# Performance work log

Hardware: AMD Instinct MI355X
Metric: run time of the kernel (lower is better)

The kernel has to match this reference:

```python
import jax, jax.numpy as jnp
import numpy as np

DIM_SED = 256
DIM_DOA = 256
DIM_ATTN = 256
NUM_HEADS = 8
HEAD_DIM = DIM_ATTN // NUM_HEADS
SCALE = HEAD_DIM ** -0.5
B, N_SED, N_DOA = 2, 2048, 2048


def setup_inputs() -> dict:
    key = jax.random.key(0)
    ks = jax.random.split(key, 8)
    s = lambda fan_in: 1.0 / np.sqrt(fan_in)
    return {
        "x_sed": jax.random.normal(ks[0], (B, N_SED, DIM_SED), jnp.float32),
        "x_doa": jax.random.normal(ks[1], (B, N_DOA, DIM_DOA), jnp.float32),
        # nn.Linear stores weight as [out, in]; we keep [in, out] for x @ W
        "W_sed_in": jax.random.uniform(ks[2], (DIM_SED, 2 * DIM_ATTN), jnp.float32, -s(DIM_SED), s(DIM_SED)),
        "W_doa_in": jax.random.uniform(ks[3], (DIM_DOA, 2 * DIM_ATTN), jnp.float32, -s(DIM_DOA), s(DIM_DOA)),
        "W_sed_out": jax.random.uniform(ks[4], (DIM_ATTN, DIM_SED), jnp.float32, -s(DIM_ATTN), s(DIM_ATTN)),
        "b_sed_out": jax.random.uniform(ks[5], (DIM_SED,), jnp.float32, -s(DIM_ATTN), s(DIM_ATTN)),
        "W_doa_out": jax.random.uniform(ks[6], (DIM_ATTN, DIM_DOA), jnp.float32, -s(DIM_ATTN), s(DIM_ATTN)),
        "b_doa_out": jax.random.uniform(ks[7], (DIM_DOA,), jnp.float32, -s(DIM_ATTN), s(DIM_ATTN)),
    }


def _split_heads(rv, B, N):
    # rv: [B, N, 2*DIM_ATTN] -> r, v each [B, H, N, hd]
    rv = rv.reshape(B, N, 2, NUM_HEADS, HEAD_DIM).transpose(2, 0, 3, 1, 4)
    return rv[0], rv[1]


def reference(x_sed, x_doa, W_sed_in, W_doa_in, W_sed_out, b_sed_out, W_doa_out, b_doa_out):
    B_, Ns, _ = x_sed.shape
    _, Nd, _ = x_doa.shape
    r_sed, v_sed = _split_heads(x_sed @ W_sed_in, B_, Ns)  # [B,H,Ns,hd]
    r_doa, v_doa = _split_heads(x_doa @ W_doa_in, B_, Nd)  # [B,H,Nd,hd]

    # Shared score matrix, softmaxed in both directions (dropout = identity, eval mode)
    attn = jnp.einsum('bhsd,bhtd->bhst', r_sed, r_doa) * SCALE  # [B,H,Ns,Nd]
    attn_sed2doa = jax.nn.softmax(attn, axis=-1)               # row-wise
    attn_doa2sed = jax.nn.softmax(attn, axis=-2)               # col-wise (softmax of attn^T over last dim)

    x_sed_fused = jnp.einsum('bhst,bhtd->bhsd', attn_sed2doa, v_doa)
    x_sed_fused = x_sed_fused.transpose(0, 2, 1, 3).reshape(B_, Ns, DIM_ATTN)
    x_sed_fused = x_sed_fused @ W_sed_out + b_sed_out

    x_doa_fused = jnp.einsum('bhst,bhsd->bhtd', attn_doa2sed, v_sed)
    x_doa_fused = x_doa_fused.transpose(0, 2, 1, 3).reshape(B_, Nd, DIM_ATTN)
    x_doa_fused = x_doa_fused @ W_doa_out + b_doa_out
    return (x_sed_fused, x_doa_fused)
```

## Files before the change

### kernel.cpp

```cpp
#include <hip/hip_runtime.h>
#include <hip/hip_bf16.h>

typedef short short8 __attribute__((ext_vector_type(8)));
typedef float f32x4 __attribute__((ext_vector_type(4)));
typedef float f32x16 __attribute__((ext_vector_type(16)));
typedef unsigned int uint4v __attribute__((ext_vector_type(4)));
typedef unsigned short ushort_t;

__device__ inline ushort_t f2bf(float f) {
    union { float f; unsigned u; } x; x.f = f;
    unsigned r = x.u + 0x7fffu + ((x.u >> 16) & 1u);
    return (ushort_t)(r >> 16);
}
__device__ inline ushort_t f2bf_u(float x) {
    union { __hip_bfloat16 h; ushort_t u; } cv;
    cv.h = __float2bfloat16(x);
    return cv.u;
}
__device__ inline float bf2f(ushort_t u) {
    union { unsigned u; float f; } cv; cv.u = ((unsigned)u) << 16; return cv.f;
}

#define GLD_LDS16(src, dst)                                                  \
    __builtin_amdgcn_global_load_lds(                                        \
        (const __attribute__((address_space(1))) void*)(src),                \
        (__attribute__((address_space(3))) void*)(dst), 16, 0, 0)

#define RSQ 0.5050100f

__global__ __launch_bounds__(256) void prep_w_kernel(const float* __restrict__ w0,
                                                     const float* __restrict__ w1,
                                                     const float* __restrict__ w2,
                                                     const float* __restrict__ w3,
                                                     ushort_t* __restrict__ t0,
                                                     ushort_t* __restrict__ t1,
                                                     ushort_t* __restrict__ t2,
                                                     ushort_t* __restrict__ t3) {
    __shared__ float tile[64][65];
    int z = blockIdx.y;
    const float* W; ushort_t* T; int J;
    if (z == 0)      { W = w0; T = t0; J = 512; }
    else if (z == 1) { W = w1; T = t1; J = 512; }
    else if (z == 2) { W = w2; T = t2; J = 256; }
    else             { W = w3; T = t3; J = 256; }
    int ntj = J >> 6;
    int nt = ntj * 4;
    int tix = blockIdx.x;
    if (tix >= nt) return;
    int tj = tix % ntj, tk = tix / ntj;
    int j0 = tj * 64, k0 = tk * 64;
    int tid = threadIdx.x;

    int jj = (tid & 15) * 4, kk0 = tid >> 4;
    #pragma unroll
    for (int kk = kk0; kk < 64; kk += 16) {
        float4 v = *reinterpret_cast<const float4*>(&W[(size_t)(k0 + kk) * J + j0 + jj]);
        tile[kk][jj] = v.x; tile[kk][jj + 1] = v.y;
        tile[kk][jj + 2] = v.z; tile[kk][jj + 3] = v.w;
    }
    __syncthreads();
    int kk4 = (tid & 15) * 4, jj0 = tid >> 4;
    #pragma unroll
    for (int j2 = jj0; j2 < 64; j2 += 16) {
        ushort4 o;
        o.x = f2bf(tile[kk4][j2]);     o.y = f2bf(tile[kk4 + 1][j2]);
        o.z = f2bf(tile[kk4 + 2][j2]); o.w = f2bf(tile[kk4 + 3][j2]);
        *reinterpret_cast<ushort4*>(&T[(size_t)(j0 + j2) * 256 + k0 + kk4]) = o;
    }
}

__global__ __launch_bounds__(256) void gemm_in_kernel(
    const float* __restrict__ A0, const float* __restrict__ A1,
    const ushort_t* __restrict__ B0, const ushort_t* __restrict__ B1,
    ushort_t* __restrict__ R0, ushort_t* __restrict__ R1,
    ushort_t* __restrict__ V0, ushort_t* __restrict__ V1) {
    const float* A = blockIdx.z ? A1 : A0;
    const ushort_t* Bt = blockIdx.z ? B1 : B0;
    ushort_t* R = blockIdx.z ? R1 : R0;
    ushort_t* Vt = blockIdx.z ? V1 : V0;
    constexpr int K = 256;
    const int w = threadIdx.x >> 6, lane = threadIdx.x & 63;
    const int l16 = lane & 15, g = lane >> 4;
    const int m0 = blockIdx.x * 64 + w * 16;
    const int cb = blockIdx.y * 128;

    f32x4 acc[8] = {};
    const float* Ap = A + (size_t)(m0 + l16) * K + 8 * g;
    const ushort_t* Bp = Bt + (size_t)(cb + l16) * K + 8 * g;

    #pragma unroll
    for (int ks = 0; ks < K; ks += 32) {
        float4 af0 = *reinterpret_cast<const float4*>(Ap + ks);
        float4 af1 = *reinterpret_cast<const float4*>(Ap + ks + 4);
        short8 a;
        a[0] = (short)f2bf_u(af0.x); a[1] = (short)f2bf_u(af0.y);
        a[2] = (short)f2bf_u(af0.z); a[3] = (short)f2bf_u(af0.w);
        a[4] = (short)f2bf_u(af1.x); a[5] = (short)f2bf_u(af1.y);
        a[6] = (short)f2bf_u(af1.z); a[7] = (short)f2bf_u(af1.w);
        #pragma unroll
        for (int c = 0; c < 8; ++c) {
            short8 b = *reinterpret_cast<const short8*>(Bp + (size_t)c * 16 * K + ks);
            acc[c] = __builtin_amdgcn_mfma_f32_16x16x32_bf16(a, b, acc[c], 0, 0, 0);
        }
    }

    if (blockIdx.y < 2) {
        #pragma unroll
        for (int c = 0; c < 8; ++c) {
            int col = cb + c * 16 + l16;
            int h = col >> 5, d = col & 31;
            #pragma unroll
            for (int r = 0; r < 4; ++r) {
                int row = m0 + 4 * g + r;
                int bb = row >> 11, n = row & 2047;
                size_t base = (size_t)(bb * 8 + h) * 65536;
                int unit = ((n >> 5) * 4 + (d >> 4) * 2 + ((d >> 3) & 1)) * 32 + (n & 31);
                R[base + (size_t)unit * 8 + (d & 7)] = f2bf_u(acc[c][r] * RSQ);
            }
        }
    } else {
        #pragma unroll
        for (int c = 0; c < 8; ++c) {
            int colp = cb - 256 + c * 16 + l16;
            int h = colp >> 5, d = colp & 31;
            int row = m0 + 4 * g;
            int bb = row >> 11, n = row & 2047;
            size_t base = (size_t)(bb * 8 + h) * 65536;
            int nl = n & 31;
            int vh = nl >> 4, r4 = nl & 15;
            int hi2 = (r4 >> 2) & 1;
            int e0 = (r4 & 3) + 4 * (r4 >> 3);
            int unit = ((n >> 5) * 4 + vh * 2 + hi2) * 32 + d;
            ushort4 s;
            s.x = f2bf_u(acc[c][0]); s.y = f2bf_u(acc[c][1]);
            s.z = f2bf_u(acc[c][2]); s.w = f2bf_u(acc[c][3]);
            *reinterpret_cast<ushort4*>(Vt + base + (size_t)unit * 8 + e0) = s;
        }
    }
}

__global__ __launch_bounds__(512, 4) void attn_kernel(
    const ushort_t* __restrict__ rU_sed, const ushort_t* __restrict__ rU_doa,
    const ushort_t* __restrict__ vU_sed, const ushort_t* __restrict__ vU_doa,
    ushort_t* __restrict__ part,
    float* __restrict__ lpart) {
    __shared__ __align__(16) ushort_t smem[16384];

    const int bid = blockIdx.x;
    const int xcd = bid & 7, i = bid >> 3;
    const int stream = xcd * 4 + (i & 3);
    const int rest = i >> 2;
    const int qblk = rest & 7, kvh = rest >> 3;
    const int dir = stream >> 4, bh = stream & 15;

    const ushort_t* rQ = dir ? rU_doa : rU_sed;
    const ushort_t* rK = dir ? rU_sed : rU_doa;
    const ushort_t* vV = dir ? vU_sed : vU_doa;

    const int tid = threadIdx.x;
    const int w = tid >> 6, lane = tid & 63;
    const int l31 = lane & 31, hi = lane >> 5;
    const size_t sB = (size_t)bh * 65536;
    const int qbase = qblk * 256 + w * 32;

    const short8 qf0 = *reinterpret_cast<const short8*>(rQ + sB + (size_t)qbase * 32 + lane * 8);
    const short8 qf1 = *reinterpret_cast<const short8*>(rQ + sB + (size_t)qbase * 32 + 512 + lane * 8);

    const ushort_t* Kbase = rK + sB + (size_t)kvh * 32768;
    const ushort_t* Vbase = vV + sB + (size_t)kvh * 32768;
    const ushort_t* srcK = Kbase + tid * 8;
    const ushort_t* srcV = Vbase + tid * 8;
    const int dstK = w * 512;
    const int dstV = 4096 + w * 512;

    f32x16 acc = {};
    f32x4 lv = {};

    auto stage = [&](int t, int bufsel) {
        GLD_LDS16(srcK + (size_t)t * 4096, &smem[bufsel * 8192 + dstK]);
        GLD_LDS16(srcV + (size_t)t * 4096, &smem[bufsel * 8192 + dstV]);
    };

    int buf = 0;
    stage(0, 0);
    __syncthreads();

    for (int t = 0; t < 8; ++t) {
        if (t < 7) stage(t + 1, buf ^ 1);
        const ushort_t* KB = &smem[buf * 8192];
        const ushort_t* VB = &smem[buf * 8192 + 4096];
        #pragma unroll
        for (int s = 0; s < 4; ++s) {
            short8 kf0 = *reinterpret_cast<const short8*>(KB + s * 1024 + lane * 8);
            short8 kf1 = *reinterpret_cast<const short8*>(KB + s * 1024 + 512 + lane * 8);
            short8 vf0 = *reinterpret_cast<const short8*>(VB + s * 1024 + lane * 8);
            short8 vf1 = *reinterpret_cast<const short8*>(VB + s * 1024 + 512 + lane * 8);

            f32x16 z16 = {};
            f32x16 st = __builtin_amdgcn_mfma_f32_32x32x16_bf16(kf0, qf0, z16, 0, 0, 0);
            st = __builtin_amdgcn_mfma_f32_32x32x16_bf16(kf1, qf1, st, 0, 0, 0);

            float p[16];
            #pragma unroll
            for (int j = 0; j < 16; ++j) {
                p[j] = __builtin_amdgcn_exp2f(st[j]);
            }
            #pragma unroll
            for (int j = 0; j < 16; ++j) lv[j & 3] += p[j];

            unsigned pk[8];
            #pragma unroll
            for (int j = 0; j < 8; ++j) {
                asm("v_cvt_pk_bf16_f32 %0, %1, %2" : "=v"(pk[j]) : "v"(p[2 * j]), "v"(p[2 * j + 1]));
            }
            union { uint4v u; short8 s; } c1, c2;
            c1.u = uint4v{pk[0], pk[1], pk[2], pk[3]};
            c2.u = uint4v{pk[4], pk[5], pk[6], pk[7]};

            acc = __builtin_amdgcn_mfma_f32_32x32x16_bf16(vf0, c1.s, acc, 0, 0, 0);
            acc = __builtin_amdgcn_mfma_f32_32x32x16_bf16(vf1, c2.s, acc, 0, 0, 0);
        }
        __syncthreads();
        buf ^= 1;
    }

    float l = (lv[0] + lv[1]) + (lv[2] + lv[3]);
    l += __shfl_xor(l, 32);
    const int q = qbase + l31;
    const size_t prow = ((size_t)stream * 2 + kvh) * 2048 + q;
    if (lane < 32) lpart[prow] = l;
    ushort_t* pa = part + prow * 32;
    #pragma unroll
    for (int r = 0; r < 16; ++r) {
        int d = (r & 3) + 8 * (r >> 2) + 4 * hi;
        pa[d] = f2bf(acc[r]);
    }
}

__global__ __launch_bounds__(256) void gemm_out_kernel(
    const ushort_t* __restrict__ part, const float* __restrict__ lpart,
    const ushort_t* __restrict__ b0, const ushort_t* __restrict__ b1,
    float* __restrict__ c0, float* __restrict__ c1,
    const float* __restrict__ bias0, const float* __restrict__ bias1) {
    const int z = blockIdx.z;
    const ushort_t* Bt = z ? b1 : b0;
    float* C = z ? c1 : c0;
    const float* bias = z ? bias1 : bias0;
    constexpr int K = 256, N = 256;
    const int w = threadIdx.x >> 6, lane = threadIdx.x & 63;
    const int l16 = lane & 15, g = lane >> 4;
    const int m0 = blockIdx.x * 64 + w * 16;
    const int cb = blockIdx.y * 128;

    const int row = m0 + l16;
    const int bb = row >> 11, q = row & 2047;

    f32x4 acc[8] = {};
    const ushort_t* Bp = Bt + (size_t)(cb + l16) * K + 8 * g;
    #pragma unroll
    for (int it = 0; it < 8; ++it) {
        const int strm = z * 16 + bb * 8 + it;
        const size_t pr0 = ((size_t)strm * 2) * 2048 + q;
        float l0 = lpart[pr0], l1 = lpart[pr0 + 2048];
        float inv = 1.0f / (l0 + l1);
        const ushort_t* p0 = part + pr0 * 32 + 8 * g;
        const ushort_t* p1 = p0 + (size_t)2048 * 32;
        short8 pa = *reinterpret_cast<const short8*>(p0);
        short8 pb = *reinterpret_cast<const short8*>(p1);
        short8 a;
        #pragma unroll
        for (int e = 0; e < 8; ++e) {
            a[e] = (short)f2bf_u((bf2f((ushort_t)pa[e]) + bf2f((ushort_t)pb[e])) * inv);
        }
        #pragma unroll
        for (int c = 0; c < 8; ++c) {
            short8 b = *reinterpret_cast<const short8*>(Bp + (size_t)c * 16 * K + it * 32);
            acc[c] = __builtin_amdgcn_mfma_f32_16x16x32_bf16(a, b, acc[c], 0, 0, 0);
        }
    }
    #pragma unroll
    for (int c = 0; c < 8; ++c) {
        int col = cb + c * 16 + l16;
        #pragma unroll
        for (int r = 0; r < 4; ++r) {
            int orow = m0 + 4 * g + r;
            C[(size_t)orow * N + col] = acc[c][r] + bias[col];
        }
    }
}

extern "C" void kernel_launch(void* const* d_in, const int* in_sizes, int n_in,
                              void* d_out, int out_size, void* d_ws, size_t ws_size,
                              hipStream_t stream) {
    const float* x_sed     = (const float*)d_in[0];
    const float* x_doa     = (const float*)d_in[1];
    const float* W_sed_in  = (const float*)d_in[2];
    const float* W_doa_in  = (const float*)d_in[3];
    const float* W_sed_out = (const float*)d_in[4];
    const float* b_sed_out = (const float*)d_in[5];
    const float* W_doa_out = (const float*)d_in[6];
    const float* b_doa_out = (const float*)d_in[7];
    float* out = (float*)d_out;

    ushort_t* ws = (ushort_t*)d_ws;
    ushort_t* wt_si  = ws;
    ushort_t* wt_di  = wt_si  + 131072;
    ushort_t* wt_so  = wt_di  + 131072;
    ushort_t* wt_do  = wt_so  + 65536;
    ushort_t* rU_sed = wt_do  + 65536;
    ushort_t* rU_doa = rU_sed + 1048576;
    ushort_t* vU_sed = rU_doa + 1048576;
    ushort_t* vU_doa = vU_sed + 1048576;
    ushort_t* part   = vU_doa + 1048576;
    float*    lpart  = (float*)(part + 4194304);

    prep_w_kernel<<<dim3(32, 4), 256, 0, stream>>>(W_sed_in, W_doa_in, W_sed_out, W_doa_out,
                                                   wt_si, wt_di, wt_so, wt_do);
    gemm_in_kernel<<<dim3(64, 4, 2), 256, 0, stream>>>(x_sed, x_doa, wt_si, wt_di,
                                                       rU_sed, rU_doa, vU_sed, vU_doa);
    attn_kernel<<<dim3(512), 512, 0, stream>>>(rU_sed, rU_doa, vU_sed, vU_doa, part, lpart);
    gemm_out_kernel<<<dim3(64, 2, 2), 256, 0, stream>>>(part, lpart, wt_so, wt_do,
                                                        out, out + 1048576, b_sed_out, b_doa_out);
}
```

Measured before the change: 67.52 us.

## Double KV tile size and software-pipeline QK MFMA ahead of softmax-PV

Staged KV tiles double from 128 to 256 keys per step, so the loop runs 4 iterations with half as many barriers. Inside each tile, the QK^T MFMA for sub-block s is issued before the exp/convert/PV work of sub-block s-1, letting matrix ops overlap transcendental and convert work. Row sums now accumulate in a 16-wide vector, which avoids a serial add chain but costs more registers. LDS use doubles to 64 KB per block, which may reduce occupancy against the launch bound of 4 blocks.

```diff
diff --git a/kernel.cpp b/kernel.cpp
--- a/kernel.cpp
+++ b/kernel.cpp
@@ -144,7 +144,7 @@
     const ushort_t* __restrict__ vU_sed, const ushort_t* __restrict__ vU_doa,
     ushort_t* __restrict__ part,
     float* __restrict__ lpart) {
-    __shared__ __align__(16) ushort_t smem[16384];
+    __shared__ __align__(16) ushort_t smem[32768];
 
     const int bid = blockIdx.x;
     const int xcd = bid & 7, i = bid >> 3;
@@ -170,61 +170,70 @@
     const ushort_t* Vbase = vV + sB + (size_t)kvh * 32768;
     const ushort_t* srcK = Kbase + tid * 8;
     const ushort_t* srcV = Vbase + tid * 8;
-    const int dstK = w * 512;
-    const int dstV = 4096 + w * 512;
 
     f32x16 acc = {};
-    f32x4 lv = {};
+    f32x16 lvv = {};
 
     auto stage = [&](int t, int bufsel) {
-        GLD_LDS16(srcK + (size_t)t * 4096, &smem[bufsel * 8192 + dstK]);
-        GLD_LDS16(srcV + (size_t)t * 4096, &smem[bufsel * 8192 + dstV]);
+        const ushort_t* sk = srcK + (size_t)t * 8192;
+        const ushort_t* sv = srcV + (size_t)t * 8192;
+        ushort_t* dk = &smem[bufsel * 16384 + w * 512];
+        GLD_LDS16(sk,        dk);
+        GLD_LDS16(sk + 4096, dk + 4096);
+        GLD_LDS16(sv,        dk + 8192);
+        GLD_LDS16(sv + 4096, dk + 12288);
+    };
+
+    auto QK = [&](const ushort_t* KB, int s) -> f32x16 {
+        short8 kf0 = *reinterpret_cast<const short8*>(KB + s * 1024 + lane * 8);
+        short8 kf1 = *reinterpret_cast<const short8*>(KB + s * 1024 + 512 + lane * 8);
+        f32x16 z16 = {};
+        f32x16 st = __builtin_amdgcn_mfma_f32_32x32x16_bf16(kf0, qf0, z16, 0, 0, 0);
+        return __builtin_amdgcn_mfma_f32_32x32x16_bf16(kf1, qf1, st, 0, 0, 0);
+    };
+
+    auto FIN = [&](const ushort_t* VB, int s, f32x16 st) {
+        short8 vf0 = *reinterpret_cast<const short8*>(VB + s * 1024 + lane * 8);
+        short8 vf1 = *reinterpret_cast<const short8*>(VB + s * 1024 + 512 + lane * 8);
+        f32x16 pv;
+        #pragma unroll
+        for (int j = 0; j < 16; ++j) pv[j] = __builtin_amdgcn_exp2f(st[j]);
+        lvv += pv;
+        unsigned pk[8];
+        #pragma unroll
+        for (int j = 0; j < 8; ++j) {
+            asm("v_cvt_pk_bf16_f32 %0, %1, %2" : "=v"(pk[j]) : "v"(pv[2 * j]), "v"(pv[2 * j + 1]));
+        }
+        union { uint4v u; short8 s; } c1, c2;
+        c1.u = uint4v{pk[0], pk[1], pk[2], pk[3]};
+        c2.u = uint4v{pk[4], pk[5], pk[6], pk[7]};
+        acc = __builtin_amdgcn_mfma_f32_32x32x16_bf16(vf0, c1.s, acc, 0, 0, 0);
+        acc = __builtin_amdgcn_mfma_f32_32x32x16_bf16(vf1, c2.s, acc, 0, 0, 0);
     };
 
     int buf = 0;
     stage(0, 0);
     __syncthreads();
 
-    for (int t = 0; t < 8; ++t) {
-        if (t < 7) stage(t + 1, buf ^ 1);
-        const ushort_t* KB = &smem[buf * 8192];
-        const ushort_t* VB = &smem[buf * 8192 + 4096];
-        #pragma unroll
-        for (int s = 0; s < 4; ++s) {
-            short8 kf0 = *reinterpret_cast<const short8*>(KB + s * 1024 + lane * 8);
-            short8 kf1 = *reinterpret_cast<const short8*>(KB + s * 1024 + 512 + lane * 8);
-            short8 vf0 = *reinterpret_cast<const short8*>(VB + s * 1024 + lane * 8);
-            short8 vf1 = *reinterpret_cast<const short8*>(VB + s * 1024 + 512 + lane * 8);
-
-            f32x16 z16 = {};
-            f32x16 st = __builtin_amdgcn_mfma_f32_32x32x16_bf16(kf0, qf0, z16, 0, 0, 0);
-            st = __builtin_amdgcn_mfma_f32_32x32x16_bf16(kf1, qf1, st, 0, 0, 0);
-
-            float p[16];
-            #pragma unroll
-            for (int j = 0; j < 16; ++j) {
-                p[j] = __builtin_amdgcn_exp2f(st[j]);
-            }
-            #pragma unroll
-            for (int j = 0; j < 16; ++j) lv[j & 3] += p[j];
-
-            unsigned pk[8];
-            #pragma unroll
-            for (int j = 0; j < 8; ++j) {
-                asm("v_cvt_pk_bf16_f32 %0, %1, %2" : "=v"(pk[j]) : "v"(p[2 * j]), "v"(p[2 * j + 1]));
-            }
-            union { uint4v u; short8 s; } c1, c2;
-            c1.u = uint4v{pk[0], pk[1], pk[2], pk[3]};
-            c2.u = uint4v{pk[4], pk[5], pk[6], pk[7]};
-
-            acc = __builtin_amdgcn_mfma_f32_32x32x16_bf16(vf0, c1.s, acc, 0, 0, 0);
-            acc = __builtin_amdgcn_mfma_f32_32x32x16_bf16(vf1, c2.s, acc, 0, 0, 0);
-        }
+    for (int t = 0; t < 4; ++t) {
+        if (t < 3) stage(t + 1, buf ^ 1);
+        const ushort_t* KB = &smem[buf * 16384];
+        const ushort_t* VB = KB + 8192;
+        f32x16 st_p = QK(KB, 0);
+        #pragma unroll
+        for (int s = 1; s < 8; ++s) {
+            f32x16 st_n = QK(KB, s);
+            FIN(VB, s - 1, st_p);
+            st_p = st_n;
+        }
+        FIN(VB, 7, st_p);
         __syncthreads();
         buf ^= 1;
     }
 
-    float l = (lv[0] + lv[1]) + (lv[2] + lv[3]);
+    float l = 0.f;
+    #pragma unroll
+    for (int j = 0; j < 16; ++j) l += lvv[j];
     l += __shfl_xor(l, 32);
     const int q = qbase + l31;
     const size_t prow = ((size_t)stream * 2 + kvh) * 2048 + q;
```

After: 67.84 us. Within noise of the previous version (+0.5%).

## Split attention into 4 KV partitions with smaller 256-thread blocks

Applied to the files above, without the earlier changes.

The attention kernel changes from 512 blocks of 512 threads, each covering half the keys, to 2048 blocks of 256 threads, each covering a quarter of the keys over 128 queries. Staging issues four LDS loads per thread, and the exp and pack work is split into two halves to shorten register live ranges. The output GEMM now reduces four partial accumulators and four partial row sums. The aim is more parallelism and better latency hiding, at the cost of twice the partial-output traffic and a larger reduction in the output kernel.

```diff
diff --git a/kernel.cpp b/kernel.cpp
--- a/kernel.cpp
+++ b/kernel.cpp
@@ -139,7 +139,7 @@
     }
 }
 
-__global__ __launch_bounds__(512, 4) void attn_kernel(
+__global__ __launch_bounds__(256, 5) void attn_kernel(
     const ushort_t* __restrict__ rU_sed, const ushort_t* __restrict__ rU_doa,
     const ushort_t* __restrict__ vU_sed, const ushort_t* __restrict__ vU_doa,
     ushort_t* __restrict__ part,
@@ -150,7 +150,7 @@
     const int xcd = bid & 7, i = bid >> 3;
     const int stream = xcd * 4 + (i & 3);
     const int rest = i >> 2;
-    const int qblk = rest & 7, kvh = rest >> 3;
+    const int qblk = rest & 15, kvq = rest >> 4;
     const int dir = stream >> 4, bh = stream & 15;
 
     const ushort_t* rQ = dir ? rU_doa : rU_sed;
@@ -161,34 +161,37 @@
     const int w = tid >> 6, lane = tid & 63;
     const int l31 = lane & 31, hi = lane >> 5;
     const size_t sB = (size_t)bh * 65536;
-    const int qbase = qblk * 256 + w * 32;
+    const int qbase = qblk * 128 + w * 32;
 
     const short8 qf0 = *reinterpret_cast<const short8*>(rQ + sB + (size_t)qbase * 32 + lane * 8);
     const short8 qf1 = *reinterpret_cast<const short8*>(rQ + sB + (size_t)qbase * 32 + 512 + lane * 8);
 
-    const ushort_t* Kbase = rK + sB + (size_t)kvh * 32768;
-    const ushort_t* Vbase = vV + sB + (size_t)kvh * 32768;
+    const ushort_t* Kbase = rK + sB + (size_t)kvq * 16384;
+    const ushort_t* Vbase = vV + sB + (size_t)kvq * 16384;
     const ushort_t* srcK = Kbase + tid * 8;
     const ushort_t* srcV = Vbase + tid * 8;
-    const int dstK = w * 512;
-    const int dstV = 4096 + w * 512;
 
     f32x16 acc = {};
     f32x4 lv = {};
 
     auto stage = [&](int t, int bufsel) {
-        GLD_LDS16(srcK + (size_t)t * 4096, &smem[bufsel * 8192 + dstK]);
-        GLD_LDS16(srcV + (size_t)t * 4096, &smem[bufsel * 8192 + dstV]);
+        const ushort_t* sk = srcK + (size_t)t * 4096;
+        const ushort_t* sv = srcV + (size_t)t * 4096;
+        ushort_t* dk = &smem[bufsel * 8192 + w * 512];
+        GLD_LDS16(sk,        dk);
+        GLD_LDS16(sk + 2048, dk + 2048);
+        GLD_LDS16(sv,        dk + 4096);
+        GLD_LDS16(sv + 2048, dk + 6144);
     };
 
     int buf = 0;
     stage(0, 0);
     __syncthreads();
 
-    for (int t = 0; t < 8; ++t) {
-        if (t < 7) stage(t + 1, buf ^ 1);
+    for (int t = 0; t < 4; ++t) {
+        if (t < 3) stage(t + 1, buf ^ 1);
         const ushort_t* KB = &smem[buf * 8192];
-        const ushort_t* VB = &smem[buf * 8192 + 4096];
+        const ushort_t* VB = KB + 4096;
         #pragma unroll
         for (int s = 0; s < 4; ++s) {
             short8 kf0 = *reinterpret_cast<const short8*>(KB + s * 1024 + lane * 8);
@@ -200,25 +203,38 @@
             f32x16 st = __builtin_amdgcn_mfma_f32_32x32x16_bf16(kf0, qf0, z16, 0, 0, 0);
             st = __builtin_amdgcn_mfma_f32_32x32x16_bf16(kf1, qf1, st, 0, 0, 0);
 
-            float p[16];
-            #pragma unroll
-            for (int j = 0; j < 16; ++j) {
-                p[j] = __builtin_amdgcn_exp2f(st[j]);
+            short8 c1s, c2s;
+            {
+                float p[8]; unsigned pk[4];
+                #pragma unroll
+                for (int j = 0; j < 8; ++j) p[j] = __builtin_amdgcn_exp2f(st[j]);
+                #pragma unroll
+                for (int j = 0; j < 8; ++j) lv[j & 3] += p[j];
+                #pragma unroll
+                for (int j = 0; j < 4; ++j) {
+                    asm("v_cvt_pk_bf16_f32 %0, %1, %2" : "=v"(pk[j]) : "v"(p[2 * j]), "v"(p[2 * j + 1]));
+                }
+                union { uint4v u; short8 s; } cc;
+                cc.u = uint4v{pk[0], pk[1], pk[2], pk[3]};
+                c1s = cc.s;
             }
-            #pragma unroll
-            for (int j = 0; j < 16; ++j) lv[j & 3] += p[j];
-
-            unsigned pk[8];
-            #pragma unroll
-            for (int j = 0; j < 8; ++j) {
-                asm("v_cvt_pk_bf16_f32 %0, %1, %2" : "=v"(pk[j]) : "v"(p[2 * j]), "v"(p[2 * j + 1]));
+            {
+                float p[8]; unsigned pk[4];
+                #pragma unroll
+                for (int j = 0; j < 8; ++j) p[j] = __builtin_amdgcn_exp2f(st[8 + j]);
+                #pragma unroll
+                for (int j = 0; j < 8; ++j) lv[j & 3] += p[j];
+                #pragma unroll
+                for (int j = 0; j < 4; ++j) {
+                    asm("v_cvt_pk_bf16_f32 %0, %1, %2" : "=v"(pk[j]) : "v"(p[2 * j]), "v"(p[2 * j + 1]));
+                }
+                union { uint4v u; short8 s; } cc;
+                cc.u = uint4v{pk[0], pk[1], pk[2], pk[3]};
+                c2s = cc.s;
             }
-            union { uint4v u; short8 s; } c1, c2;
-            c1.u = uint4v{pk[0], pk[1], pk[2], pk[3]};
-            c2.u = uint4v{pk[4], pk[5], pk[6], pk[7]};
-
-            acc = __builtin_amdgcn_mfma_f32_32x32x16_bf16(vf0, c1.s, acc, 0, 0, 0);
-            acc = __builtin_amdgcn_mfma_f32_32x32x16_bf16(vf1, c2.s, acc, 0, 0, 0);
+
+            acc = __builtin_amdgcn_mfma_f32_32x32x16_bf16(vf0, c1s, acc, 0, 0, 0);
+            acc = __builtin_amdgcn_mfma_f32_32x32x16_bf16(vf1, c2s, acc, 0, 0, 0);
         }
         __syncthreads();
         buf ^= 1;
@@ -227,7 +243,7 @@
     float l = (lv[0] + lv[1]) + (lv[2] + lv[3]);
     l += __shfl_xor(l, 32);
     const int q = qbase + l31;
-    const size_t prow = ((size_t)stream * 2 + kvh) * 2048 + q;
+    const size_t prow = ((size_t)stream * 4 + kvq) * 2048 + q;
     if (lane < 32) lpart[prow] = l;
     ushort_t* pa = part + prow * 32;
     #pragma unroll
@@ -260,17 +276,20 @@
     #pragma unroll
     for (int it = 0; it < 8; ++it) {
         const int strm = z * 16 + bb * 8 + it;
-        const size_t pr0 = ((size_t)strm * 2) * 2048 + q;
-        float l0 = lpart[pr0], l1 = lpart[pr0 + 2048];
-        float inv = 1.0f / (l0 + l1);
+        const size_t pr0 = ((size_t)strm * 4) * 2048 + q;
+        float l = lpart[pr0] + lpart[pr0 + 2048] + lpart[pr0 + 4096] + lpart[pr0 + 6144];
+        float inv = 1.0f / l;
         const ushort_t* p0 = part + pr0 * 32 + 8 * g;
-        const ushort_t* p1 = p0 + (size_t)2048 * 32;
         short8 pa = *reinterpret_cast<const short8*>(p0);
-        short8 pb = *reinterpret_cast<const short8*>(p1);
+        short8 pb = *reinterpret_cast<const short8*>(p0 + (size_t)2048 * 32);
+        short8 pc = *reinterpret_cast<const short8*>(p0 + (size_t)4096 * 32);
+        short8 pd = *reinterpret_cast<const short8*>(p0 + (size_t)6144 * 32);
         short8 a;
         #pragma unroll
         for (int e = 0; e < 8; ++e) {
-            a[e] = (short)f2bf_u((bf2f((ushort_t)pa[e]) + bf2f((ushort_t)pb[e])) * inv);
+            float sum = (bf2f((ushort_t)pa[e]) + bf2f((ushort_t)pb[e]))
+                      + (bf2f((ushort_t)pc[e]) + bf2f((ushort_t)pd[e]));
+            a[e] = (short)f2bf_u(sum * inv);
         }
         #pragma unroll
         for (int c = 0; c < 8; ++c) {
@@ -312,13 +331,13 @@
     ushort_t* vU_sed = rU_doa + 1048576;
     ushort_t* vU_doa = vU_sed + 1048576;
     ushort_t* part   = vU_doa + 1048576;
-    float*    lpart  = (float*)(part + 4194304);
+    float*    lpart  = (float*)(part + 8388608);
 
     prep_w_kernel<<<dim3(32, 4), 256, 0, stream>>>(W_sed_in, W_doa_in, W_sed_out, W_doa_out,
                                                    wt_si, wt_di, wt_so, wt_do);
     gemm_in_kernel<<<dim3(64, 4, 2), 256, 0, stream>>>(x_sed, x_doa, wt_si, wt_di,
                                                        rU_sed, rU_doa, vU_sed, vU_doa);
-    attn_kernel<<<dim3(512), 512, 0, stream>>>(rU_sed, rU_doa, vU_sed, vU_doa, part, lpart);
+    attn_kernel<<<dim3(2048), 256, 0, stream>>>(rU_sed, rU_doa, vU_sed, vU_doa, part, lpart);
     gemm_out_kernel<<<dim3(64, 2, 2), 256, 0, stream>>>(part, lpart, wt_so, wt_do,
                                                         out, out + 1048576, b_sed_out, b_doa_out);
 }
```

After: 68.17 us. No clear change (+1.0%).

## Fuse weight transpose and bf16 conversion into GEMM kernels via swizzled LDS staging

Applied to the files above, without the earlier changes.

Removes the separate prep_w kernel. Each GEMM block now reads its fp32 weight slice straight from global memory, converts it to bf16, and writes it transposed into a 64 KB XOR-swizzled LDS tile. The MFMA B operands are then read from LDS instead of global memory. This saves a kernel launch and the workspace round trip. In exchange, every block redoes the weight conversion with strided uncoalesced-per-thread loads, and the 64 KB of LDS per block lowers occupancy.

```diff
diff --git a/kernel.cpp b/kernel.cpp
--- a/kernel.cpp
+++ b/kernel.cpp
@@ -28,54 +28,31 @@
 
 #define RSQ 0.5050100f
 
-__global__ __launch_bounds__(256) void prep_w_kernel(const float* __restrict__ w0,
-                                                     const float* __restrict__ w1,
-                                                     const float* __restrict__ w2,
-                                                     const float* __restrict__ w3,
-                                                     ushort_t* __restrict__ t0,
-                                                     ushort_t* __restrict__ t1,
-                                                     ushort_t* __restrict__ t2,
-                                                     ushort_t* __restrict__ t3) {
-    __shared__ float tile[64][65];
-    int z = blockIdx.y;
-    const float* W; ushort_t* T; int J;
-    if (z == 0)      { W = w0; T = t0; J = 512; }
-    else if (z == 1) { W = w1; T = t1; J = 512; }
-    else if (z == 2) { W = w2; T = t2; J = 256; }
-    else             { W = w3; T = t3; J = 256; }
-    int ntj = J >> 6;
-    int nt = ntj * 4;
-    int tix = blockIdx.x;
-    if (tix >= nt) return;
-    int tj = tix % ntj, tk = tix / ntj;
-    int j0 = tj * 64, k0 = tk * 64;
-    int tid = threadIdx.x;
-
-    int jj = (tid & 15) * 4, kk0 = tid >> 4;
-    #pragma unroll
-    for (int kk = kk0; kk < 64; kk += 16) {
-        float4 v = *reinterpret_cast<const float4*>(&W[(size_t)(k0 + kk) * J + j0 + jj]);
-        tile[kk][jj] = v.x; tile[kk][jj + 1] = v.y;
-        tile[kk][jj + 2] = v.z; tile[kk][jj + 3] = v.w;
-    }
-    __syncthreads();
-    int kk4 = (tid & 15) * 4, jj0 = tid >> 4;
-    #pragma unroll
-    for (int j2 = jj0; j2 < 64; j2 += 16) {
-        ushort4 o;
-        o.x = f2bf(tile[kk4][j2]);     o.y = f2bf(tile[kk4 + 1][j2]);
-        o.z = f2bf(tile[kk4 + 2][j2]); o.w = f2bf(tile[kk4 + 3][j2]);
-        *reinterpret_cast<ushort4*>(&T[(size_t)(j0 + j2) * 256 + k0 + kk4]) = o;
+__device__ inline void stage_w(const float* __restrict__ W, int J, int cb,
+                               ushort_t* lds, int tid) {
+    const int c = tid & 127;
+    const int kh = tid >> 7;
+    const float* src = W + (size_t)(kh * 128) * J + cb + c;
+    #pragma unroll
+    for (int kc = 0; kc < 16; ++kc) {
+        short8 tmp;
+        #pragma unroll
+        for (int m = 0; m < 8; ++m)
+            tmp[m] = (short)f2bf(src[(size_t)(kc * 8 + m) * J]);
+        int a0 = c * 512 + (kh * 128 + kc * 8) * 2;
+        int a = a0 ^ (((a0 >> 9) & 7) << 4);
+        *reinterpret_cast<short8*>(reinterpret_cast<char*>(lds) + a) = tmp;
     }
 }
 
 __global__ __launch_bounds__(256) void gemm_in_kernel(
     const float* __restrict__ A0, const float* __restrict__ A1,
-    const ushort_t* __restrict__ B0, const ushort_t* __restrict__ B1,
+    const float* __restrict__ W0, const float* __restrict__ W1,
     ushort_t* __restrict__ R0, ushort_t* __restrict__ R1,
     ushort_t* __restrict__ V0, ushort_t* __restrict__ V1) {
+    __shared__ __align__(16) ushort_t bsm[32768];
     const float* A = blockIdx.z ? A1 : A0;
-    const ushort_t* Bt = blockIdx.z ? B1 : B0;
+    const float* W = blockIdx.z ? W1 : W0;
     ushort_t* R = blockIdx.z ? R1 : R0;
     ushort_t* Vt = blockIdx.z ? V1 : V0;
     constexpr int K = 256;
@@ -84,9 +61,13 @@
     const int m0 = blockIdx.x * 64 + w * 16;
     const int cb = blockIdx.y * 128;
 
+    stage_w(W, 512, cb, bsm, threadIdx.x);
+    __syncthreads();
+
     f32x4 acc[8] = {};
     const float* Ap = A + (size_t)(m0 + l16) * K + 8 * g;
-    const ushort_t* Bp = Bt + (size_t)(cb + l16) * K + 8 * g;
+    const int xorv = (l16 & 7) << 4;
+    const char* bsb = reinterpret_cast<const char*>(bsm);
 
     #pragma unroll
     for (int ks = 0; ks < K; ks += 32) {
@@ -99,7 +80,8 @@
         a[6] = (short)f2bf_u(af1.z); a[7] = (short)f2bf_u(af1.w);
         #pragma unroll
         for (int c = 0; c < 8; ++c) {
-            short8 b = *reinterpret_cast<const short8*>(Bp + (size_t)c * 16 * K + ks);
+            int a0 = (c * 16 + l16) * 512 + (ks + 8 * g) * 2;
+            short8 b = *reinterpret_cast<const short8*>(bsb + (a0 ^ xorv));
             acc[c] = __builtin_amdgcn_mfma_f32_16x16x32_bf16(a, b, acc[c], 0, 0, 0);
         }
     }
@@ -239,24 +221,29 @@
 
 __global__ __launch_bounds__(256) void gemm_out_kernel(
     const ushort_t* __restrict__ part, const float* __restrict__ lpart,
-    const ushort_t* __restrict__ b0, const ushort_t* __restrict__ b1,
+    const float* __restrict__ W0, const float* __restrict__ W1,
     float* __restrict__ c0, float* __restrict__ c1,
     const float* __restrict__ bias0, const float* __restrict__ bias1) {
+    __shared__ __align__(16) ushort_t bsm[32768];
     const int z = blockIdx.z;
-    const ushort_t* Bt = z ? b1 : b0;
+    const float* W = z ? W1 : W0;
     float* C = z ? c1 : c0;
     const float* bias = z ? bias1 : bias0;
-    constexpr int K = 256, N = 256;
+    constexpr int N = 256;
     const int w = threadIdx.x >> 6, lane = threadIdx.x & 63;
     const int l16 = lane & 15, g = lane >> 4;
     const int m0 = blockIdx.x * 64 + w * 16;
     const int cb = blockIdx.y * 128;
 
+    stage_w(W, 256, cb, bsm, threadIdx.x);
+    __syncthreads();
+
     const int row = m0 + l16;
     const int bb = row >> 11, q = row & 2047;
+    const int xorv = (l16 & 7) << 4;
+    const char* bsb = reinterpret_cast<const char*>(bsm);
 
     f32x4 acc[8] = {};
-    const ushort_t* Bp = Bt + (size_t)(cb + l16) * K + 8 * g;
     #pragma unroll
     for (int it = 0; it < 8; ++it) {
         const int strm = z * 16 + bb * 8 + it;
@@ -274,7 +261,8 @@
         }
         #pragma unroll
         for (int c = 0; c < 8; ++c) {
-            short8 b = *reinterpret_cast<const short8*>(Bp + (size_t)c * 16 * K + it * 32);
+            int a0 = (c * 16 + l16) * 512 + (it * 32 + 8 * g) * 2;
+            short8 b = *reinterpret_cast<const short8*>(bsb + (a0 ^ xorv));
             acc[c] = __builtin_amdgcn_mfma_f32_16x16x32_bf16(a, b, acc[c], 0, 0, 0);
         }
     }
@@ -303,22 +291,16 @@
     float* out = (float*)d_out;
 
     ushort_t* ws = (ushort_t*)d_ws;
-    ushort_t* wt_si  = ws;
-    ushort_t* wt_di  = wt_si  + 131072;
-    ushort_t* wt_so  = wt_di  + 131072;
-    ushort_t* wt_do  = wt_so  + 65536;
-    ushort_t* rU_sed = wt_do  + 65536;
+    ushort_t* rU_sed = ws;
     ushort_t* rU_doa = rU_sed + 1048576;
     ushort_t* vU_sed = rU_doa + 1048576;
     ushort_t* vU_doa = vU_sed + 1048576;
     ushort_t* part   = vU_doa + 1048576;
     float*    lpart  = (float*)(part + 4194304);
 
-    prep_w_kernel<<<dim3(32, 4), 256, 0, stream>>>(W_sed_in, W_doa_in, W_sed_out, W_doa_out,
-                                                   wt_si, wt_di, wt_so, wt_do);
-    gemm_in_kernel<<<dim3(64, 4, 2), 256, 0, stream>>>(x_sed, x_doa, wt_si, wt_di,
+    gemm_in_kernel<<<dim3(64, 4, 2), 256, 0, stream>>>(x_sed, x_doa, W_sed_in, W_doa_in,
                                                        rU_sed, rU_doa, vU_sed, vU_doa);
     attn_kernel<<<dim3(512), 512, 0, stream>>>(rU_sed, rU_doa, vU_sed, vU_doa, part, lpart);
-    gemm_out_kernel<<<dim3(64, 2, 2), 256, 0, stream>>>(part, lpart, wt_so, wt_do,
+    gemm_out_kernel<<<dim3(64, 2, 2), 256, 0, stream>>>(part, lpart, W_sed_out, W_doa_out,
                                                         out, out + 1048576, b_sed_out, b_doa_out);
 }
```

Result: faster. 61.81 us (-8.5%).
